# Optimization experiments

Measured on AMD Instinct MI355X. Metric: run time of the kernel, lower is better.

Reference implementation:

```python
import jax, jax.numpy as jnp
import numpy as np

GROUPS = 8      # hard-coded in module
SUBNET = 3     # A.shape[0]
BN_EPS = 1e-5  # torch BatchNorm2d default eps


def _batchnorm(y, gamma):
    # training-mode BatchNorm2d with weight=gamma, bias=0 (per bn_init)
    mean = jnp.mean(y, axis=(0, 2, 3), keepdims=True)
    var = jnp.var(y, axis=(0, 2, 3), keepdims=True)  # biased, as torch uses for normalization
    return gamma * (y - mean) * jax.lax.rsqrt(var + BN_EPS)


def setup_inputs() -> dict:
    key = jax.random.key(0)
    k1, k2, k3 = jax.random.split(key, 3)
    x = jax.random.normal(k1, (64, 64, 288, 19), dtype=jnp.float32)          # [N, C, T, V]
    DecoupleA = jax.random.normal(k2, (SUBNET, GROUPS, 19, 19), dtype=jnp.float32)
    std = float(np.sqrt(0.5 / 192.0))  # normal_(0, sqrt(0.5/(out_ch*subnet)))
    Linear_weight = jax.random.normal(k3, (64, 192), dtype=jnp.float32) * std  # [C_in, subnet*C_out]
    Linear_bias = jnp.full((1, 192, 1, 1), 1e-6, dtype=jnp.float32)
    return {"x": x, "DecoupleA": DecoupleA, "Linear_weight": Linear_weight, "Linear_bias": Linear_bias}


def reference(x, DecoupleA, Linear_weight, Linear_bias):
    n, c_in, t, v = x.shape
    out_ch = Linear_weight.shape[1] // SUBNET

    # DecoupleA.repeat(1, out_ch // groups, 1, 1) -> tile channel dim
    learn_A = jnp.tile(DecoupleA, (1, out_ch // GROUPS, 1, 1))  # [3, out_ch, V, V]
    # per-subnet L2 norm over the channel dim (dim=1), +1e-4
    norm = jnp.sqrt(jnp.sum(learn_A * learn_A, axis=1, keepdims=True)) + 1e-4
    norm_learn_A = learn_A / norm  # [3, out_ch, V, V]

    # linear projection over channels: nctw,cd->ndtw
    y = jnp.einsum('nctw,cd->ndtw', x, Linear_weight) + Linear_bias  # [N, 3*out_ch, T, V]
    y = _batchnorm(y, 1.0)  # bn0: weight=1, bias=0

    y = y.reshape(n, SUBNET, out_ch, t, v)
    # per-channel adjacency contraction over joints
    y = jnp.einsum('nkctv,kcvw->nctw', y, norm_learn_A)  # [N, out_ch, T, V]
    y = _batchnorm(y, 1e-6)  # bn: weight initialized to 1e-6

    y = y + x  # down() is identity since in_channels == out_channels
    return jax.nn.relu(y)
```

## Files before the change

kernel.cpp:

```cpp
#include <hip/hip_runtime.h>
#include <math.h>

#define NN 64
#define CC 64
#define TDIM 288
#define VV 19
#define DD 192
#define SS (TDIM*VV)
#define MSAMP (NN*SS)

#define WS_S    0
#define WS_MU   4096
#define WS_ZSUM 4160
#define WS_ZSS  4224
#define WS_BETA 4288
#define WS_WP   4480
#define WS_AP   16768
#define WS_ZSC  25432
#define WS_ZSH  25496
#define WS_Z    25600

typedef __attribute__((ext_vector_type(8))) short short8;
typedef __attribute__((ext_vector_type(4))) float f32x4;

__device__ __forceinline__ short f2bf(float f) {
    unsigned u = __float_as_uint(f);
    u = (u + 0x7FFFu + ((u >> 16) & 1u)) >> 16;
    return (short)u;
}

__global__ __launch_bounds__(256, 4) void k1_cov(const float* __restrict__ x,
                                                 float* __restrict__ ws) {
    __shared__ short Xk[6144];
    const int tid = threadIdx.x;
    const int wv = tid >> 6, lane = tid & 63;
    const int lrow = lane & 15, lgrp = lane >> 4;
    const int cs = tid >> 2, jq = tid & 3;

    f32x4 acc[4];
#pragma unroll
    for (int ct = 0; ct < 4; ++ct)
#pragma unroll
        for (int r = 0; r < 4; ++r) acc[ct][r] = 0.f;
    float mu = 0.f;

    for (int i = 0; i < 8; ++i) {
        const int cid = blockIdx.x * 8 + i;
        const int nn = cid / 57;
        const int off = (cid - nn * 57) * 96;
        const float* xp = x + (size_t)nn * (CC * SS) + (size_t)cs * SS + off + jq * 24;
        __syncthreads();
#pragma unroll
        for (int u = 0; u < 6; ++u) {
            const float4 v = *(const float4*)&xp[u * 4];
            mu += (v.x + v.y) + (v.z + v.w);
            const int j = jq * 24 + u * 4;
            const int base = (j >> 3) * 512 + cs * 8 + (j & 7);
            *(unsigned*)&Xk[base]     = (unsigned)(unsigned short)f2bf(v.x) |
                                        ((unsigned)(unsigned short)f2bf(v.y) << 16);
            *(unsigned*)&Xk[base + 2] = (unsigned)(unsigned short)f2bf(v.z) |
                                        ((unsigned)(unsigned short)f2bf(v.w) << 16);
        }
        __syncthreads();
#pragma unroll
        for (int ks = 0; ks < 3; ++ks) {
            const short8 a = *(const short8*)&Xk[(ks * 4 + lgrp) * 512 + (wv * 16 + lrow) * 8];
#pragma unroll
            for (int ct = 0; ct < 4; ++ct) {
                const short8 b = *(const short8*)&Xk[(ks * 4 + lgrp) * 512 + (ct * 16 + lrow) * 8];
                acc[ct] = __builtin_amdgcn_mfma_f32_16x16x32_bf16(a, b, acc[ct], 0, 0, 0);
            }
        }
    }
    mu += __shfl_down(mu, 1);
    mu += __shfl_down(mu, 2);
    if ((tid & 3) == 0) atomicAdd(&ws[WS_MU + cs], mu);
#pragma unroll
    for (int ct = 0; ct < 4; ++ct)
#pragma unroll
        for (int r = 0; r < 4; ++r)
            atomicAdd(&ws[WS_S + (wv * 16 + lgrp * 4 + r) * 64 + ct * 16 + lrow],
                      acc[ct][r]);
}

__global__ __launch_bounds__(256) void k2_prep(const float* __restrict__ A,
                                               const float* __restrict__ W,
                                               const float* __restrict__ bias,
                                               float* __restrict__ ws) {
    const int tid = threadIdx.x;
    if (blockIdx.x == 3) {
        for (int f = tid; f < 3 * 19 * 19; f += 256) {
            const int k = f / 361, vw = f % 361;
            const int v = vw / 19, w2 = vw % 19;
            float ssq = 0.f;
            for (int g = 0; g < 8; ++g) {
                const float a = A[((k * 8 + g) * 19 + v) * 19 + w2];
                ssq = fmaf(a, a, ssq);
            }
            const float inv = 1.0f / (sqrtf(8.0f * ssq) + 1e-4f);
            for (int g = 0; g < 8; ++g)
                ws[WS_AP + ((k * 8 + g) * 19 + v) * 19 + w2] =
                    A[((k * 8 + g) * 19 + v) * 19 + w2] * inv;
        }
        return;
    }
    __shared__ float Sn[64][64];
    __shared__ float mun[64];
    const float invM = 1.0f / (float)MSAMP;
    for (int f = tid; f < 4096; f += 256) Sn[f >> 6][f & 63] = ws[WS_S + f] * invM;
    if (tid < 64) mun[tid] = ws[WS_MU + tid] * invM;
    __syncthreads();
    if (tid < 64) {
        const int d = blockIdx.x * 64 + tid;
        float w[64];
#pragma unroll
        for (int c = 0; c < 64; ++c) w[c] = W[c * DD + d];
        float wmu = 0.f;
#pragma unroll
        for (int c = 0; c < 64; ++c) wmu = fmaf(w[c], mun[c], wmu);
        float q = 0.f;
#pragma unroll
        for (int c = 0; c < 64; ++c) {
            float t0 = 0.f, t1 = 0.f, t2 = 0.f, t3 = 0.f;
#pragma unroll
            for (int c2 = 0; c2 < 64; c2 += 4) {
                t0 = fmaf(Sn[c][c2 + 0], w[c2 + 0], t0);
                t1 = fmaf(Sn[c][c2 + 1], w[c2 + 1], t1);
                t2 = fmaf(Sn[c][c2 + 2], w[c2 + 2], t2);
                t3 = fmaf(Sn[c][c2 + 3], w[c2 + 3], t3);
            }
            q = fmaf(w[c], (t0 + t1) + (t2 + t3), q);
        }
        const float var = q - wmu * wmu;
        const float rs = rsqrtf(var + 1e-5f);
        ws[WS_BETA + d] = -wmu * rs;
#pragma unroll
        for (int c = 0; c < 64; ++c) ws[WS_WP + c * DD + d] = w[c] * rs;
    }
}

__global__ __launch_bounds__(256, 3) void k3_main(const float* __restrict__ x,
                                                  float* __restrict__ ws) {
    __shared__ short Xs[5120];
    __shared__ short Y2[16384];
    const int tid = threadIdx.x;
    const int wv = tid >> 6, lane = tid & 63;
    const int lrow = lane & 15, lgrp = lane >> 4;
    const int n = blockIdx.y;
    const int sb0 = blockIdx.x * 16 * 19;

    {
        const int g = tid >> 5, m = tid & 31;
        const int base = g * 2048 + 7 * 256 + m * 8;
#pragma unroll
        for (int e = 1; e < 8; ++e) Y2[base + e] = 0;
    }

    short8 WpB[3][2];
    float betaR[3];
#pragma unroll
    for (int nt = 0; nt < 3; ++nt) {
        const int d = (wv * 3 + nt) * 16 + lrow;
        betaR[nt] = ws[WS_BETA + d];
#pragma unroll
        for (int ks = 0; ks < 2; ++ks) {
            short8 tm;
#pragma unroll
            for (int e = 0; e < 8; ++e) {
                const int c = ks * 32 + lgrp * 8 + e;
                tm[e] = f2bf(ws[WS_WP + c * DD + d]);
            }
            WpB[nt][ks] = tm;
        }
    }
    short8 ApB[2][2][2];
#pragma unroll
    for (int gi = 0; gi < 2; ++gi) {
        const int g = wv * 2 + gi;
#pragma unroll
        for (int nt = 0; nt < 2; ++nt) {
            const int w2 = nt * 16 + lrow;
#pragma unroll
            for (int ks = 0; ks < 2; ++ks) {
                short8 tm;
#pragma unroll
                for (int e = 0; e < 8; ++e) {
                    const int q = ks * 32 + lgrp * 8 + e;
                    short val = 0;
                    if (q < 57 && w2 < 19) {
                        const int k = q / 19, v = q - k * 19;
                        val = f2bf(ws[WS_AP + ((k * 8 + g) * 19 + v) * 19 + w2]);
                    }
                    tm[e] = val;
                }
                ApB[gi][nt][ks] = tm;
            }
        }
    }

    const float* xb = x + (size_t)n * (CC * SS);
    float* zb = ws + WS_Z + (size_t)n * (CC * SS);
    const int cs = tid >> 2, jq = tid & 3;

    for (int sc = 0; sc < 4; ++sc) {
        const int sb = sb0 + sc * 76;
        __syncthreads();
        {
            const float* xp = xb + (size_t)cs * SS + sb + jq * 19;
            const int bi = (cs >> 3) * 640 + (cs & 7);
#pragma unroll
            for (int jj = 0; jj < 19; ++jj)
                Xs[bi + (jq * 19 + jj) * 8] = f2bf(xp[jj]);
        }
        __syncthreads();
#pragma unroll
        for (int mt = 0; mt < 5; ++mt) {
            const short8 a0 = *(const short8*)&Xs[(0 + lgrp) * 640 + (mt * 16 + lrow) * 8];
            const short8 a1 = *(const short8*)&Xs[(4 + lgrp) * 640 + (mt * 16 + lrow) * 8];
            const int j0 = mt * 16 + lgrp * 4;
#pragma unroll
            for (int nt = 0; nt < 3; ++nt) {
                f32x4 acc = {0.f, 0.f, 0.f, 0.f};
                acc = __builtin_amdgcn_mfma_f32_16x16x32_bf16(a0, WpB[nt][0], acc, 0, 0, 0);
                acc = __builtin_amdgcn_mfma_f32_16x16x32_bf16(a1, WpB[nt][1], acc, 0, 0, 0);
                const int d = (wv * 3 + nt) * 16 + lrow;
                const int k = d >> 6, c2 = d & 63;
                const int g = c2 & 7, c8 = c2 >> 3;
#pragma unroll
                for (int r = 0; r < 4; ++r) {
                    const int j = j0 + r;
                    if (j < 76) {
                        const int t = (j * 27) >> 9;
                        const int v = j - t * 19;
                        const int q = k * 19 + v;
                        Y2[g * 2048 + (q >> 3) * 256 + (c8 * 4 + t) * 8 + (q & 7)] =
                            f2bf(acc[r] + betaR[nt]);
                    }
                }
            }
        }
        __syncthreads();
#pragma unroll
        for (int gi = 0; gi < 2; ++gi) {
            const int g = wv * 2 + gi;
#pragma unroll
            for (int mt = 0; mt < 2; ++mt) {
                const short8 a0 = *(const short8*)&Y2[g * 2048 + (0 + lgrp) * 256 + (mt * 16 + lrow) * 8];
                const short8 a1 = *(const short8*)&Y2[g * 2048 + (4 + lgrp) * 256 + (mt * 16 + lrow) * 8];
                f32x4 acc0 = {0.f, 0.f, 0.f, 0.f};
                f32x4 acc1 = {0.f, 0.f, 0.f, 0.f};
                acc0 = __builtin_amdgcn_mfma_f32_16x16x32_bf16(a0, ApB[gi][0][0], acc0, 0, 0, 0);
                acc0 = __builtin_amdgcn_mfma_f32_16x16x32_bf16(a1, ApB[gi][0][1], acc0, 0, 0, 0);
                acc1 = __builtin_amdgcn_mfma_f32_16x16x32_bf16(a0, ApB[gi][1][0], acc1, 0, 0, 0);
                acc1 = __builtin_amdgcn_mfma_f32_16x16x32_bf16(a1, ApB[gi][1][1], acc1, 0, 0, 0);
#pragma unroll
                for (int r = 0; r < 4; ++r) {
                    const int m = mt * 16 + lgrp * 4 + r;
                    const int c = (m >> 2) * 8 + g;
                    const size_t s = (size_t)c * SS + sb + (m & 3) * 19;
                    zb[s + lrow] = acc0[r];
                    if (lrow < 3) zb[s + 16 + lrow] = acc1[r];
                }
            }
        }
    }
}

__global__ __launch_bounds__(256) void k4a_zred(float* __restrict__ ws) {
    const int bid = blockIdx.x;
    const float* zp = ws + WS_Z + (size_t)bid * SS;
    float s = 0.f, q = 0.f;
    for (int i = threadIdx.x; i < SS / 4; i += 256) {
        const float4 v = *(const float4*)&zp[i * 4];
        s += (v.x + v.y) + (v.z + v.w);
        q += fmaf(v.x, v.x, fmaf(v.y, v.y, fmaf(v.z, v.z, v.w * v.w)));
    }
#pragma unroll
    for (int o = 32; o; o >>= 1) { s += __shfl_down(s, o); q += __shfl_down(q, o); }
    __shared__ float rs[4], rq[4];
    if ((threadIdx.x & 63) == 0) { rs[threadIdx.x >> 6] = s; rq[threadIdx.x >> 6] = q; }
    __syncthreads();
    if (threadIdx.x == 0) {
        s = (rs[0] + rs[1]) + (rs[2] + rs[3]);
        q = (rq[0] + rq[1]) + (rq[2] + rq[3]);
        atomicAdd(&ws[WS_ZSUM + (bid & 63)], s);
        atomicAdd(&ws[WS_ZSS + (bid & 63)], q);
    }
}

__global__ void k4b_final(float* __restrict__ ws) {
    const int c = threadIdx.x;
    if (c < 64) {
        const float invM = 1.0f / (float)MSAMP;
        const float m = ws[WS_ZSUM + c] * invM;
        const float e2 = ws[WS_ZSS + c] * invM;
        const float var = e2 - m * m;
        const float sc = 1e-6f * rsqrtf(var + 1e-5f);
        ws[WS_ZSC + c] = sc;
        ws[WS_ZSH + c] = -m * sc;
    }
}

__global__ __launch_bounds__(256) void k5_final(const float* __restrict__ x,
                                                const float* __restrict__ ws,
                                                float* __restrict__ out) {
    __shared__ float sc[64], sh[64];
    if (threadIdx.x < 64) {
        sc[threadIdx.x] = ws[WS_ZSC + threadIdx.x];
        sh[threadIdx.x] = ws[WS_ZSH + threadIdx.x];
    }
    __syncthreads();
    const float* z = ws + WS_Z;
    const int total4 = (NN * CC * SS) / 4;
    for (int i4 = blockIdx.x * 256 + threadIdx.x; i4 < total4;
         i4 += gridDim.x * 256) {
        const int i = i4 * 4;
        const int c = (i / SS) & 63;
        const float4 xv = *(const float4*)&x[i];
        const float4 zv = *(const float4*)&z[i];
        float4 o;
        o.x = fmaxf(fmaf(zv.x, sc[c], sh[c]) + xv.x, 0.f);
        o.y = fmaxf(fmaf(zv.y, sc[c], sh[c]) + xv.y, 0.f);
        o.z = fmaxf(fmaf(zv.z, sc[c], sh[c]) + xv.z, 0.f);
        o.w = fmaxf(fmaf(zv.w, sc[c], sh[c]) + xv.w, 0.f);
        *(float4*)&out[i] = o;
    }
}

extern "C" void kernel_launch(void* const* d_in, const int* in_sizes, int n_in,
                              void* d_out, int out_size, void* d_ws, size_t ws_size,
                              hipStream_t stream) {
    (void)in_sizes; (void)n_in; (void)out_size; (void)ws_size;
    const float* x    = (const float*)d_in[0];
    const float* A    = (const float*)d_in[1];
    const float* W    = (const float*)d_in[2];
    const float* bias = (const float*)d_in[3];
    float* out = (float*)d_out;
    float* ws  = (float*)d_ws;

    hipMemsetAsync(d_ws, 0, WS_BETA * sizeof(float), stream);

    k1_cov   <<<456, 256, 0, stream>>>(x, ws);
    k2_prep  <<<4,   256, 0, stream>>>(A, W, bias, ws);
    k3_main  <<<dim3(18, 64), 256, 0, stream>>>(x, ws);
    k4a_zred <<<4096, 256, 0, stream>>>(ws);
    k4b_final<<<1,    64, 0, stream>>>(ws);
    k5_final <<<2048, 256, 0, stream>>>(x, ws, out);
}
```

Measured before the change: 328.9 us.

## Fuse z statistics into main kernel, store z as bf16, swizzle Y2 LDS

Per-channel sum and sum-of-squares of z are now accumulated in registers inside k3_main, reduced with lane shuffles and added atomically, so the separate k4a_zred pass that re-read all of z is removed. The z intermediate is stored as bf16 instead of fp32, which halves the write traffic in k3 and the read traffic in k5_final. The Y2 shared-memory tile index is XOR-swizzled by group to reduce LDS bank conflicts. The trade-offs are bf16 rounding of z before the final normalization and more atomics into the stats buffers.

```diff
diff --git a/kernel.cpp b/kernel.cpp
--- a/kernel.cpp
+++ b/kernel.cpp
@@ -27,6 +27,9 @@
     unsigned u = __float_as_uint(f);
     u = (u + 0x7FFFu + ((u >> 16) & 1u)) >> 16;
     return (short)u;
+}
+__device__ __forceinline__ float bf2f(unsigned short h) {
+    return __uint_as_float((unsigned)h << 16);
 }
 
 __global__ __launch_bounds__(256, 4) void k1_cov(const float* __restrict__ x,
@@ -199,8 +202,11 @@
     }
 
     const float* xb = x + (size_t)n * (CC * SS);
-    float* zb = ws + WS_Z + (size_t)n * (CC * SS);
+    unsigned short* zbh = (unsigned short*)(ws + WS_Z) + (size_t)n * (CC * SS);
     const int cs = tid >> 2, jq = tid & 3;
+
+    float zsA[2][2]  = {{0.f, 0.f}, {0.f, 0.f}};
+    float zssA[2][2] = {{0.f, 0.f}, {0.f, 0.f}};
 
     for (int sc = 0; sc < 4; ++sc) {
         const int sb = sb0 + sc * 76;
@@ -233,7 +239,8 @@
                         const int t = (j * 27) >> 9;
                         const int v = j - t * 19;
                         const int q = k * 19 + v;
-                        Y2[g * 2048 + (q >> 3) * 256 + (c8 * 4 + t) * 8 + (q & 7)] =
+                        const int m = c8 * 4 + t;
+                        Y2[g * 2048 + (q >> 3) * 256 + (m ^ g) * 8 + (q & 7)] =
                             f2bf(acc[r] + betaR[nt]);
                     }
                 }
@@ -245,8 +252,9 @@
             const int g = wv * 2 + gi;
 #pragma unroll
             for (int mt = 0; mt < 2; ++mt) {
-                const short8 a0 = *(const short8*)&Y2[g * 2048 + (0 + lgrp) * 256 + (mt * 16 + lrow) * 8];
-                const short8 a1 = *(const short8*)&Y2[g * 2048 + (4 + lgrp) * 256 + (mt * 16 + lrow) * 8];
+                const int mrow = mt * 16 + lrow;
+                const short8 a0 = *(const short8*)&Y2[g * 2048 + (0 + lgrp) * 256 + (mrow ^ g) * 8];
+                const short8 a1 = *(const short8*)&Y2[g * 2048 + (4 + lgrp) * 256 + (mrow ^ g) * 8];
                 f32x4 acc0 = {0.f, 0.f, 0.f, 0.f};
                 f32x4 acc1 = {0.f, 0.f, 0.f, 0.f};
                 acc0 = __builtin_amdgcn_mfma_f32_16x16x32_bf16(a0, ApB[gi][0][0], acc0, 0, 0, 0);
@@ -258,34 +266,35 @@
                     const int m = mt * 16 + lgrp * 4 + r;
                     const int c = (m >> 2) * 8 + g;
                     const size_t s = (size_t)c * SS + sb + (m & 3) * 19;
-                    zb[s + lrow] = acc0[r];
-                    if (lrow < 3) zb[s + 16 + lrow] = acc1[r];
+                    const float zv0 = acc0[r];
+                    zbh[s + lrow] = (unsigned short)f2bf(zv0);
+                    zsA[mt][gi] += zv0;
+                    zssA[mt][gi] = fmaf(zv0, zv0, zssA[mt][gi]);
+                    if (lrow < 3) {
+                        const float zv1 = acc1[r];
+                        zbh[s + 16 + lrow] = (unsigned short)f2bf(zv1);
+                        zsA[mt][gi] += zv1;
+                        zssA[mt][gi] = fmaf(zv1, zv1, zssA[mt][gi]);
+                    }
                 }
             }
         }
     }
-}
-
-__global__ __launch_bounds__(256) void k4a_zred(float* __restrict__ ws) {
-    const int bid = blockIdx.x;
-    const float* zp = ws + WS_Z + (size_t)bid * SS;
-    float s = 0.f, q = 0.f;
-    for (int i = threadIdx.x; i < SS / 4; i += 256) {
-        const float4 v = *(const float4*)&zp[i * 4];
-        s += (v.x + v.y) + (v.z + v.w);
-        q += fmaf(v.x, v.x, fmaf(v.y, v.y, fmaf(v.z, v.z, v.w * v.w)));
-    }
-#pragma unroll
-    for (int o = 32; o; o >>= 1) { s += __shfl_down(s, o); q += __shfl_down(q, o); }
-    __shared__ float rs[4], rq[4];
-    if ((threadIdx.x & 63) == 0) { rs[threadIdx.x >> 6] = s; rq[threadIdx.x >> 6] = q; }
-    __syncthreads();
-    if (threadIdx.x == 0) {
-        s = (rs[0] + rs[1]) + (rs[2] + rs[3]);
-        q = (rq[0] + rq[1]) + (rq[2] + rq[3]);
-        atomicAdd(&ws[WS_ZSUM + (bid & 63)], s);
-        atomicAdd(&ws[WS_ZSS + (bid & 63)], q);
-    }
+#pragma unroll
+    for (int mt = 0; mt < 2; ++mt)
+#pragma unroll
+        for (int gi = 0; gi < 2; ++gi) {
+            float s = zsA[mt][gi], q = zssA[mt][gi];
+            s += __shfl_xor(s, 1); q += __shfl_xor(q, 1);
+            s += __shfl_xor(s, 2); q += __shfl_xor(q, 2);
+            s += __shfl_xor(s, 4); q += __shfl_xor(q, 4);
+            s += __shfl_xor(s, 8); q += __shfl_xor(q, 8);
+            if (lrow == 0) {
+                const int c = (mt * 4 + lgrp) * 8 + wv * 2 + gi;
+                atomicAdd(&ws[WS_ZSUM + c], s);
+                atomicAdd(&ws[WS_ZSS + c], q);
+            }
+        }
 }
 
 __global__ void k4b_final(float* __restrict__ ws) {
@@ -310,19 +319,19 @@
         sh[threadIdx.x] = ws[WS_ZSH + threadIdx.x];
     }
     __syncthreads();
-    const float* z = ws + WS_Z;
+    const unsigned short* zh = (const unsigned short*)(ws + WS_Z);
     const int total4 = (NN * CC * SS) / 4;
     for (int i4 = blockIdx.x * 256 + threadIdx.x; i4 < total4;
          i4 += gridDim.x * 256) {
         const int i = i4 * 4;
         const int c = (i / SS) & 63;
         const float4 xv = *(const float4*)&x[i];
-        const float4 zv = *(const float4*)&z[i];
+        const ushort4 zv = *(const ushort4*)&zh[i];
         float4 o;
-        o.x = fmaxf(fmaf(zv.x, sc[c], sh[c]) + xv.x, 0.f);
-        o.y = fmaxf(fmaf(zv.y, sc[c], sh[c]) + xv.y, 0.f);
-        o.z = fmaxf(fmaf(zv.z, sc[c], sh[c]) + xv.z, 0.f);
-        o.w = fmaxf(fmaf(zv.w, sc[c], sh[c]) + xv.w, 0.f);
+        o.x = fmaxf(fmaf(bf2f(zv.x), sc[c], sh[c]) + xv.x, 0.f);
+        o.y = fmaxf(fmaf(bf2f(zv.y), sc[c], sh[c]) + xv.y, 0.f);
+        o.z = fmaxf(fmaf(bf2f(zv.z), sc[c], sh[c]) + xv.z, 0.f);
+        o.w = fmaxf(fmaf(bf2f(zv.w), sc[c], sh[c]) + xv.w, 0.f);
         *(float4*)&out[i] = o;
     }
 }
@@ -343,7 +352,6 @@
     k1_cov   <<<456, 256, 0, stream>>>(x, ws);
     k2_prep  <<<4,   256, 0, stream>>>(A, W, bias, ws);
     k3_main  <<<dim3(18, 64), 256, 0, stream>>>(x, ws);
-    k4a_zred <<<4096, 256, 0, stream>>>(ws);
     k4b_final<<<1,    64, 0, stream>>>(ws);
     k5_final <<<2048, 256, 0, stream>>>(x, ws, out);
 }
```

New measurement: 475.8 us. 1.45x slower.
